# Performance work log

Measured on AMD Instinct MI355X. Metric: run time of the kernel, lower is better.

Reference implementation:

```python
import jax, jax.numpy as jnp
import numpy as np

N = 4096      # nodes
F = 64        # feature dim (= in = hidden = out channels)
DEPTH = 3
RATIO = 0.5


def _gcn(x, A, W, b):
    # GCNConv(improved=True): self-loop weight 2.0, sym-normalized propagation
    n = A.shape[0]
    A_hat = A + 2.0 * jnp.eye(n, dtype=A.dtype)
    deg = A_hat.sum(axis=1)
    dinv = jnp.where(deg > 0, jax.lax.rsqrt(deg), 0.0)
    A_norm = dinv[:, None] * A_hat * dinv[None, :]
    return A_norm @ (x @ W) + b


def _augment(A):
    # add_self_loops (fill 1.0) -> spspmm(A,A) -> remove_self_loops, dense form
    n = A.shape[0]
    eye = jnp.eye(n, dtype=A.dtype)
    A_sl = A + eye
    A2 = A_sl @ A_sl
    return A2 * (1.0 - eye)


def _topk_pool(x, A, p, ratio):
    # TopKPooling: score = tanh((x @ p)/||p||); keep top ceil(ratio*N) nodes
    score = jnp.tanh((x @ p) / jnp.linalg.norm(p))
    k = int(np.ceil(ratio * x.shape[0]))          # static
    vals, perm = jax.lax.top_k(score, k)
    x_new = x[perm] * vals[:, None]
    A_new = A[perm][:, perm]                      # filter_adj
    return x_new, A_new, perm


def setup_inputs() -> dict:
    key = jax.random.key(0)
    ks = jax.random.split(key, 9)
    x = jax.random.normal(ks[0], (N, F), dtype=jnp.float32)
    # sparse random undirected graph, avg degree ~32, no self loops
    u = jax.random.uniform(ks[1], (N, N), dtype=jnp.float32)
    m = (u < (16.0 / N)).astype(jnp.float32)
    adj = jnp.maximum(m, m.T) * (1.0 - jnp.eye(N, dtype=jnp.float32))
    s = 1.0 / np.sqrt(F)
    down_W = jax.random.normal(ks[2], (DEPTH + 1, F, F), dtype=jnp.float32) * s
    down_b = jnp.zeros((DEPTH + 1, F), dtype=jnp.float32)
    pool_w = jax.random.normal(ks[3], (DEPTH, F), dtype=jnp.float32) * s
    up_W = jax.random.normal(ks[4], (DEPTH, F, F), dtype=jnp.float32) * s
    up_b = jnp.zeros((DEPTH, F), dtype=jnp.float32)
    fc_w = jax.random.normal(ks[5], (F, 1), dtype=jnp.float32) * s
    fc_b = jnp.zeros((1,), dtype=jnp.float32)
    prob = jnp.zeros((), dtype=jnp.float32)  # dropout p = 0 -> deterministic
    return {"x": x, "adj": adj, "prob": prob, "down_W": down_W,
            "down_b": down_b, "pool_w": pool_w, "up_W": up_W,
            "up_b": up_b, "fc_w": fc_w, "fc_b": fc_b}


def reference(x, adj, prob, down_W, down_b, pool_w, up_W, up_b, fc_w, fc_b):
    act = jax.nn.relu
    A = adj
    h = act(_gcn(x, A, down_W[0], down_b[0]))
    xs, As, perms = [h], [A], []
    for i in range(DEPTH):
        A = _augment(A)
        h, A, perm = _topk_pool(h, A, pool_w[i], RATIO)
        h = act(_gcn(h, A, down_W[i + 1], down_b[i + 1]))
        if i < DEPTH - 1:
            xs.append(h); As.append(A)
        perms.append(perm)
    for i in range(DEPTH):
        j = DEPTH - 1 - i
        res, A, perm = xs[j], As[j], perms[j]
        up = jnp.zeros_like(res).at[perm].set(h)   # scatter unpool
        h = res + up                               # sum_res
        h = _gcn(h, A, up_W[i], up_b[i])
        if i < DEPTH - 1:
            h = act(h)
    h = jax.nn.relu(h)
    h = h / (1.0 - prob)   # dropout with p=prob(=0): all-ones keep mask
    return h @ fc_w + fc_b
```

## Files before the change

### kernel.cpp

```cpp
#include <hip/hip_runtime.h>
#include <cstdint>
#include <cstddef>


typedef float  f4v    __attribute__((ext_vector_type(4)));
typedef float  f32x4  __attribute__((ext_vector_type(4)));
typedef __bf16 bf16x8 __attribute__((ext_vector_type(8)));
typedef __bf16 bf16x4 __attribute__((ext_vector_type(4)));
typedef int    i32x4  __attribute__((ext_vector_type(4)));

#define NN0 4096
#define NN1 2048
#define NN2 1024
#define NN3 512

__global__ __launch_bounds__(256) void k_zs_deg(const float* __restrict__ X,
                                                const float* __restrict__ W,
                                                const float* __restrict__ A,
                                                int n,
                                                float* __restrict__ DEG,
                                                float* __restrict__ zs,
                                                __bf16* __restrict__ ADJB,
                                                __bf16* __restrict__ Zt0,
                                                __bf16* __restrict__ Zt1,
                                                __bf16* __restrict__ Zt2) {
    __shared__ float Ws[64][65];
    __shared__ float Xs[4][64];
    __shared__ float degs[4];
    int tid = threadIdx.x;
#pragma unroll
    for (int q = 0; q < 16; q++) {
        int idx = q * 256 + tid;
        Ws[idx >> 6][idx & 63] = W[idx];
    }
    int row0 = blockIdx.x << 2;
    int r = tid >> 6, lane = tid & 63;
    const float* ar = A + (size_t)(row0 + r) * n;
    __bf16* ab = ADJB + (size_t)(row0 + r) * n;
    float s = 0.f;
    for (int j = lane << 2; j < n; j += 256) {
        f4v a = *(const f4v*)(ar + j);
        s += a[0] + a[1] + a[2] + a[3];
        bf16x4 b;
#pragma unroll
        for (int e = 0; e < 4; e++) b[e] = (__bf16)a[e];
        *(bf16x4*)(ab + j) = b;
    }
#pragma unroll
    for (int off = 32; off > 0; off >>= 1) s += __shfl_xor(s, off);
    if (lane == 0) { degs[r] = s; DEG[row0 + r] = s; }
    Xs[r][lane] = X[((size_t)(row0 + r) << 6) + lane];
    __syncthreads();
    float acc = 0.f;
#pragma unroll
    for (int k = 0; k < 64; k++) acc = fmaf(Xs[r][k], Ws[k][lane], acc);
    float di = 1.0f / sqrtf(degs[r] + 2.0f);
    float zval = di * acc;
    zs[((size_t)(row0 + r) << 6) + lane] = zval;
    __syncthreads();
    Xs[r][lane] = zval;
    __syncthreads();
    int c = tid >> 2, rr = tid & 3;
    float v = Xs[rr][c];
    float v0 = (float)(__bf16)v;
    float v1 = (float)(__bf16)(v - v0);
    size_t o = (size_t)c * n + row0 + rr;
    Zt0[o] = (__bf16)v0;
    Zt1[o] = (__bf16)(v - v0);
    Zt2[o] = (__bf16)(v - v0 - v1);
}

__global__ __launch_bounds__(256) void k_zs_pool(const float* __restrict__ H,
                                                 const float* __restrict__ sc,
                                                 const int* __restrict__ perm,
                                                 const float* __restrict__ W,
                                                 const float* __restrict__ deg,
                                                 float* __restrict__ zs,
                                                 __bf16* __restrict__ Zt0,
                                                 __bf16* __restrict__ Zt1,
                                                 __bf16* __restrict__ Zt2,
                                                 int n) {
    __shared__ float Ws[64][65];
    __shared__ float Xs[4][64];
    int tid = threadIdx.x;
#pragma unroll
    for (int q = 0; q < 16; q++) {
        int idx = q * 256 + tid;
        Ws[idx >> 6][idx & 63] = W[idx];
    }
    int row0 = blockIdx.x << 2;
    int r = tid >> 6, f = tid & 63;
    int src = perm[row0 + r];
    Xs[r][f] = H[((size_t)src << 6) + f] * sc[src];
    __syncthreads();
    float acc = 0.f;
#pragma unroll
    for (int k = 0; k < 64; k++) acc = fmaf(Xs[r][k], Ws[k][f], acc);
    float di = 1.0f / sqrtf(deg[row0 + r] + 2.0f);
    float zval = di * acc;
    zs[((size_t)(row0 + r) << 6) + f] = zval;
    if (Zt0) {
        __syncthreads();
        Xs[r][f] = zval;
        __syncthreads();
        int c = tid >> 2, rr = tid & 3;
        float v = Xs[rr][c];
        float v0 = (float)(__bf16)v;
        float v1 = (float)(__bf16)(v - v0);
        size_t o = (size_t)c * n + row0 + rr;
        Zt0[o] = (__bf16)v0;
        Zt1[o] = (__bf16)(v - v0);
        if (Zt2) Zt2[o] = (__bf16)(v - v0 - v1);
    }
}

__global__ __launch_bounds__(256) void k_zs_unpool(const float* __restrict__ RES,
                                                   const float* __restrict__ HS,
                                                   const int* __restrict__ inv,
                                                   const float* __restrict__ W,
                                                   const float* __restrict__ deg,
                                                   float* __restrict__ zs,
                                                   __bf16* __restrict__ Zt0,
                                                   __bf16* __restrict__ Zt1,
                                                   __bf16* __restrict__ Zt2,
                                                   int n) {
    __shared__ float Ws[64][65];
    __shared__ float Xs[4][64];
    int tid = threadIdx.x;
#pragma unroll
    for (int q = 0; q < 16; q++) {
        int idx = q * 256 + tid;
        Ws[idx >> 6][idx & 63] = W[idx];
    }
    int row0 = blockIdx.x << 2;
    int r = tid >> 6, f = tid & 63;
    int grow = row0 + r;
    int iv = inv[grow];
    float xv = RES[((size_t)grow << 6) + f];
    if (iv >= 0) xv += HS[((size_t)iv << 6) + f];
    Xs[r][f] = xv;
    __syncthreads();
    float acc = 0.f;
#pragma unroll
    for (int k = 0; k < 64; k++) acc = fmaf(Xs[r][k], Ws[k][f], acc);
    float di = 1.0f / sqrtf(deg[grow] + 2.0f);
    float zval = di * acc;
    zs[((size_t)grow << 6) + f] = zval;
    if (Zt0) {
        __syncthreads();
        Xs[r][f] = zval;
        __syncthreads();
        int c = tid >> 2, rr = tid & 3;
        float v = Xs[rr][c];
        float v0 = (float)(__bf16)v;
        float v1 = (float)(__bf16)(v - v0);
        size_t o = (size_t)c * n + row0 + rr;
        Zt0[o] = (__bf16)v0;
        Zt1[o] = (__bf16)(v - v0);
        if (Zt2) Zt2[o] = (__bf16)(v - v0 - v1);
    }
}

__global__ __launch_bounds__(256) void k_prop(const float* __restrict__ A,
                                              const float* __restrict__ zs,
                                              float* __restrict__ ypart, int n) {
    int rb = blockIdx.x, ks = blockIdx.y;
    int chunk = n >> 2;
    int j0 = ks * chunk;
    __shared__ float AtT[64][68];
    __shared__ float Zt[64][68];
    int tid = threadIdx.x;
    int lr = tid >> 2;
    int lc = (tid & 3) << 4;
    int ty = tid >> 4, tx = tid & 15;
    float acc[4][4] = {};
    const float* Arow = A + (size_t)(rb * 64 + lr) * n;
    for (int jt = j0; jt < j0 + chunk; jt += 64) {
#pragma unroll
        for (int q = 0; q < 4; q++) {
            f4v av = *(const f4v*)(Arow + jt + lc + (q << 2));
#pragma unroll
            for (int e = 0; e < 4; e++) AtT[lc + (q << 2) + e][lr] = av[e];
        }
#pragma unroll
        for (int q = 0; q < 4; q++) {
            f4v zv = *(const f4v*)(zs + (((size_t)(jt + lr)) << 6) + lc + (q << 2));
            *(f4v*)&Zt[lr][lc + (q << 2)] = zv;
        }
        __syncthreads();
#pragma unroll 4
        for (int k = 0; k < 64; k++) {
            f4v a4 = *(const f4v*)&AtT[k][ty << 2];
            f4v z4 = *(const f4v*)&Zt[k][tx << 2];
#pragma unroll
            for (int r = 0; r < 4; r++)
#pragma unroll
                for (int c = 0; c < 4; c++)
                    acc[r][c] = fmaf(a4[r], z4[c], acc[r][c]);
        }
        __syncthreads();
    }
    float* yp = ypart + ((size_t)ks * n << 6);
#pragma unroll
    for (int r = 0; r < 4; r++) {
        f4v o; o[0] = acc[r][0]; o[1] = acc[r][1]; o[2] = acc[r][2]; o[3] = acc[r][3];
        *(f4v*)(yp + (((size_t)(rb * 64 + (ty << 2) + r)) << 6) + (tx << 2)) = o;
    }
}

template<int NP>
__global__ __launch_bounds__(256) void k_propm(const __bf16* __restrict__ Zt0,
                                               const __bf16* __restrict__ Zt1,
                                               const __bf16* __restrict__ Zt2,
                                               const __bf16* __restrict__ Ab,
                                               float* __restrict__ ypart,
                                               int n, int chunk) {
    __shared__ __bf16 At[128 * 64];
    __shared__ __bf16 B[NP][64 * 64];
    const __bf16* Zp[3] = {Zt0, Zt1, Zt2};
    int tid = threadIdx.x;
    int m0 = blockIdx.x * 128;
    int k0b = blockIdx.y * chunk;
    int wave = tid >> 6, lane = tid & 63, quad = lane >> 4, l16 = lane & 15;
    int wm = wave << 5;
    f32x4 acc[2][4] = {};
    for (int k0 = k0b; k0 < k0b + chunk; k0 += 64) {
#pragma unroll
        for (int it = 0; it < 4; it++) {
            int e = it * 256 + tid;
            int row = e >> 3, seg = e & 7;
            int sg = seg ^ (row & 7);
            const __bf16* g = Ab + ((size_t)(m0 + row) * n + k0 + (sg << 3));
            __builtin_amdgcn_global_load_lds(
                (const __attribute__((address_space(1))) void*)g,
                (__attribute__((address_space(3))) void*)(At + (e << 3)), 16, 0, 0);
        }
#pragma unroll
        for (int it = 0; it < 2; it++) {
            int e = it * 256 + tid;
            int row = e >> 3, seg = e & 7;
            int sg = seg ^ (row & 7);
            size_t off = (size_t)row * n + k0 + (sg << 3);
#pragma unroll
            for (int p = 0; p < NP; p++)
                __builtin_amdgcn_global_load_lds(
                    (const __attribute__((address_space(1))) void*)(Zp[p] + off),
                    (__attribute__((address_space(3))) void*)(B[p] + (e << 3)), 16, 0, 0);
        }
        __syncthreads();
#pragma unroll
        for (int kk = 0; kk < 2; kk++) {
            int s = (kk << 2) + quad;
            bf16x8 af[2];
#pragma unroll
            for (int im = 0; im < 2; im++) {
                int row = wm + (im << 4) + l16;
                af[im] = *(const bf16x8*)(At + (row << 6) + ((s ^ (row & 7)) << 3));
            }
#pragma unroll
            for (int cg = 0; cg < 4; cg++) {
                int brow = (cg << 4) + l16;
                int so = (s ^ (brow & 7)) << 3;
#pragma unroll
                for (int p = 0; p < NP; p++) {
                    bf16x8 bv = *(const bf16x8*)(B[p] + (brow << 6) + so);
#pragma unroll
                    for (int im = 0; im < 2; im++)
                        acc[im][cg] = __builtin_amdgcn_mfma_f32_16x16x32_bf16(
                            af[im], bv, acc[im][cg], 0, 0, 0);
                }
            }
        }
        __syncthreads();
    }
    float* yp = ypart + ((size_t)blockIdx.y * n << 6);
#pragma unroll
    for (int im = 0; im < 2; im++)
#pragma unroll
        for (int cg = 0; cg < 4; cg++)
#pragma unroll
            for (int r = 0; r < 4; r++) {
                int grow = m0 + wm + (im << 4) + (quad << 2) + r;
                int gcol = (cg << 4) + l16;
                yp[((size_t)grow << 6) + gcol] = acc[im][cg][r];
            }
}

__global__ __launch_bounds__(256) void k_epi(const float* __restrict__ ypart,
                                             const float* __restrict__ zs,
                                             const float* __restrict__ deg,
                                             const float* __restrict__ b,
                                             float* __restrict__ H, int n, int S,
                                             int relu,
                                             const float* __restrict__ p,
                                             float* __restrict__ score,
                                             int* __restrict__ cnt,
                                             const float* __restrict__ fcw,
                                             const float* __restrict__ fcb,
                                             const float* __restrict__ prob,
                                             float* __restrict__ out) {
    int idx = blockIdx.x * 256 + threadIdx.x;
    int i = idx >> 6, f = idx & 63;
    size_t stride = (size_t)n << 6;
    float y = 0.f;
    for (int s2 = 0; s2 < S; s2++) y += ypart[(size_t)s2 * stride + idx];
    float di = 1.0f / sqrtf(deg[i] + 2.0f);
    float v = di * (y + 2.0f * zs[idx]) + b[f];
    if (relu) v = fmaxf(v, 0.f);
    if (H) H[idx] = v;
    if (p) {
        float pv = p[f];
        float d = v * pv, q = pv * pv;
#pragma unroll
        for (int off = 32; off > 0; off >>= 1) {
            d += __shfl_xor(d, off);
            q += __shfl_xor(q, off);
        }
        if (f == 0) score[i] = tanhf(d / sqrtf(q));
        if (idx < n) cnt[idx] = 0;
    }
    if (fcw) {
        float hv = fmaxf(v, 0.f) * fcw[f];
#pragma unroll
        for (int off = 32; off > 0; off >>= 1) hv += __shfl_xor(hv, off);
        if (f == 0) out[i] = hv / (1.0f - prob[0]) + fcb[0];
    }
}

__global__ __launch_bounds__(256) void k_topk_count(const float* __restrict__ score,
                                                    int* __restrict__ cnt, int n) {
    __shared__ float sc[256];
    int j0 = blockIdx.y * 256;
    sc[threadIdx.x] = score[j0 + threadIdx.x];
    int i = blockIdx.x * 256 + threadIdx.x;
    float si = score[i];
    __syncthreads();
    int c = 0;
#pragma unroll 8
    for (int t = 0; t < 256; t++) {
        float sj = sc[t];
        int j = j0 + t;
        c += ((sj > si) || (sj == si && j < i)) ? 1 : 0;
    }
    atomicAdd(&cnt[i], c);
}
__global__ __launch_bounds__(256) void k_topk_scatter(const int* __restrict__ cnt,
                                                      int* __restrict__ perm,
                                                      int* __restrict__ inv,
                                                      float* __restrict__ degN,
                                                      int k) {
    int i = blockIdx.x * 256 + threadIdx.x;
    int c = cnt[i];
    if (c < k) perm[c] = i;
    inv[i] = (c < k) ? c : -1;
    if (i < k) degN[i] = 0.f;
}

__global__ __launch_bounds__(256) void k_gather8b(const __bf16* __restrict__ Ab,
                                                  const int* __restrict__ perm,
                                                  signed char* __restrict__ Mg,
                                                  int kbits4 ) {
    size_t idx16 = (size_t)blockIdx.x * 256 + threadIdx.x;
    int r = (int)(idx16 >> kbits4);
    int c = ((int)idx16 & ((1 << kbits4) - 1)) << 4;
    int K = 1 << (kbits4 + 4);
    int src = perm[r];
    const __bf16* rowp = Ab + (size_t)src * K + c;
    bf16x8 a0 = *(const bf16x8*)rowp;
    bf16x8 a1 = *(const bf16x8*)(rowp + 8);
    union { signed char ch[16]; i32x4 v; } u;
#pragma unroll
    for (int j = 0; j < 8; j++) {
        float val = (float)a0[j];
        if (src == c + j) val += 1.0f;
        u.ch[j] = (signed char)val;
    }
#pragma unroll
    for (int j = 0; j < 8; j++) {
        float val = (float)a1[j];
        if (src == c + 8 + j) val += 1.0f;
        u.ch[8 + j] = (signed char)val;
    }
    *(i32x4*)(Mg + (idx16 << 4)) = u.v;
}

__global__ __launch_bounds__(256) void k_gather(const float* __restrict__ A,
                                                const int* __restrict__ perm,
                                                __bf16* __restrict__ Mg,
                                                int kbits3 ) {
    size_t idx8 = (size_t)blockIdx.x * 256 + threadIdx.x;
    int r = (int)(idx8 >> kbits3);
    int c = ((int)idx8 & ((1 << kbits3) - 1)) << 3;
    int K = 1 << (kbits3 + 3);
    int src = perm[r];
    const float* rowp = A + (size_t)src * K + c;
    f4v v0 = *(const f4v*)rowp;
    f4v v1 = *(const f4v*)(rowp + 4);
    bf16x8 t;
#pragma unroll
    for (int j = 0; j < 4; j++) {
        float v = v0[j]; if (src == c + j) v += 1.0f; t[j] = (__bf16)v;
    }
#pragma unroll
    for (int j = 0; j < 4; j++) {
        float v = v1[j]; if (src == c + 4 + j) v += 1.0f; t[4 + j] = (__bf16)v;
    }
    *(bf16x8*)(Mg + idx8 * 8) = t;
}

template<int BN>
__global__ __launch_bounds__(256) void k_augmm_i8(const signed char* __restrict__ Mg,
                                                  float* __restrict__ C,
                                                  __bf16* __restrict__ Cb,
                                                  float* __restrict__ DEG,
                                                  int nk, int K) {
    __shared__ signed char At[64 * 128];
    __shared__ signed char Bt[BN * 128];
    constexpr int NI = BN / 32;
    int tid = threadIdx.x;
    int m0 = blockIdx.x * 64, n0 = blockIdx.y * BN;
    int wave = tid >> 6, lane = tid & 63;
    int wm = (wave >> 1) << 5;
    int wn = (wave & 1) * (BN >> 1);
    int quad = lane >> 4, l16 = lane & 15;
    i32x4 acc[2][NI] = {};
    for (int k0 = 0; k0 < K; k0 += 128) {
#pragma unroll
        for (int it = 0; it < 2; it++) {
            int e = it * 256 + tid;
            int row = e >> 3, cs = e & 7;
            int cg = cs ^ (row & 7);
            const signed char* g = Mg + ((size_t)(m0 + row) * K + k0 + (cg << 4));
            __builtin_amdgcn_global_load_lds(
                (const __attribute__((address_space(1))) void*)g,
                (__attribute__((address_space(3))) void*)(At + (e << 4)), 16, 0, 0);
        }
#pragma unroll
        for (int it = 0; it < BN / 32; it++) {
            int e = it * 256 + tid;
            int row = e >> 3, cs = e & 7;
            int cg = cs ^ (row & 7);
            const signed char* g = Mg + ((size_t)(n0 + row) * K + k0 + (cg << 4));
            __builtin_amdgcn_global_load_lds(
                (const __attribute__((address_space(1))) void*)g,
                (__attribute__((address_space(3))) void*)(Bt + (e << 4)), 16, 0, 0);
        }
        __syncthreads();
#pragma unroll
        for (int h = 0; h < 2; h++) {
            int cix = (h << 2) + quad;
            i32x4 af[2], bf[NI];
#pragma unroll
            for (int im = 0; im < 2; im++) {
                int row = wm + (im << 4) + l16;
                af[im] = *(const i32x4*)(At + (row << 7) + ((cix ^ (row & 7)) << 4));
            }
#pragma unroll
            for (int in2 = 0; in2 < NI; in2++) {
                int row = wn + (in2 << 4) + l16;
                bf[in2] = *(const i32x4*)(Bt + (row << 7) + ((cix ^ (row & 7)) << 4));
            }
#pragma unroll
            for (int im = 0; im < 2; im++)
#pragma unroll
                for (int in2 = 0; in2 < NI; in2++)
                    acc[im][in2] = __builtin_amdgcn_mfma_i32_16x16x64_i8(
                        af[im], bf[in2], acc[im][in2], 0, 0, 0);
        }
        __syncthreads();
    }
#pragma unroll
    for (int im = 0; im < 2; im++) {
#pragma unroll
        for (int r = 0; r < 4; r++) {
            int grow = m0 + wm + (im << 4) + (quad << 2) + r;
            int part = 0;
#pragma unroll
            for (int in2 = 0; in2 < NI; in2++) {
                int gcol = n0 + wn + (in2 << 4) + l16;
                int v = (grow == gcol) ? 0 : acc[im][in2][r];
                if (C)  C[(size_t)grow * nk + gcol] = (float)v;
                if (Cb) Cb[(size_t)grow * nk + gcol] = (__bf16)(float)v;
                part += v;
            }
#pragma unroll
            for (int off = 8; off > 0; off >>= 1) part += __shfl_xor(part, off);
            if (l16 == 0) atomicAdd(&DEG[grow], (float)part);
        }
    }
}

__global__ __launch_bounds__(256) void k_augmm_bf(const __bf16* __restrict__ Mg,
                                                  float* __restrict__ C,
                                                  float* __restrict__ DEG,
                                                  int nk, int K) {
    constexpr int BN = 64;
    __shared__ __bf16 At[64 * 64];
    __shared__ __bf16 Bt[BN * 64];
    constexpr int NI = BN / 32;
    int tid = threadIdx.x;
    int m0 = blockIdx.x * 64, n0 = blockIdx.y * BN;
    int wave = tid >> 6, lane = tid & 63;
    int wm = (wave >> 1) << 5;
    int wn = (wave & 1) * (BN >> 1);
    int quad = lane >> 4, l16 = lane & 15;
    f32x4 acc[2][NI] = {};
    for (int k0 = 0; k0 < K; k0 += 64) {
#pragma unroll
        for (int it = 0; it < 2; it++) {
            int e = it * 256 + tid;
            int row = e >> 3, seg = e & 7;
            int sg = seg ^ (row & 7);
            const __bf16* g = Mg + ((size_t)(m0 + row) * K + k0 + (sg << 3));
            __builtin_amdgcn_global_load_lds(
                (const __attribute__((address_space(1))) void*)g,
                (__attribute__((address_space(3))) void*)(At + (e << 3)), 16, 0, 0);
        }
#pragma unroll
        for (int it = 0; it < BN / 32; it++) {
            int e = it * 256 + tid;
            int row = e >> 3, seg = e & 7;
            int sg = seg ^ (row & 7);
            const __bf16* g = Mg + ((size_t)(n0 + row) * K + k0 + (sg << 3));
            __builtin_amdgcn_global_load_lds(
                (const __attribute__((address_space(1))) void*)g,
                (__attribute__((address_space(3))) void*)(Bt + (e << 3)), 16, 0, 0);
        }
        __syncthreads();
#pragma unroll
        for (int kk = 0; kk < 2; kk++) {
            int s = (kk << 2) + quad;
            bf16x8 af[2], bfm[NI];
#pragma unroll
            for (int im = 0; im < 2; im++) {
                int row = wm + (im << 4) + l16;
                af[im] = *(const bf16x8*)(At + (row << 6) + ((s ^ (row & 7)) << 3));
            }
#pragma unroll
            for (int in2 = 0; in2 < NI; in2++) {
                int row = wn + (in2 << 4) + l16;
                bfm[in2] = *(const bf16x8*)(Bt + (row << 6) + ((s ^ (row & 7)) << 3));
            }
#pragma unroll
            for (int im = 0; im < 2; im++)
#pragma unroll
                for (int in2 = 0; in2 < NI; in2++)
                    acc[im][in2] = __builtin_amdgcn_mfma_f32_16x16x32_bf16(
                        af[im], bfm[in2], acc[im][in2], 0, 0, 0);
        }
        __syncthreads();
    }
#pragma unroll
    for (int im = 0; im < 2; im++) {
#pragma unroll
        for (int r = 0; r < 4; r++) {
            int grow = m0 + wm + (im << 4) + (quad << 2) + r;
            float part = 0.f;
#pragma unroll
            for (int in2 = 0; in2 < NI; in2++) {
                int gcol = n0 + wn + (in2 << 4) + l16;
                float v = (grow == gcol) ? 0.f : acc[im][in2][r];
                C[(size_t)grow * nk + gcol] = v;
                part += v;
            }
#pragma unroll
            for (int off = 8; off > 0; off >>= 1) part += __shfl_xor(part, off);
            if (l16 == 0) atomicAdd(&DEG[grow], part);
        }
    }
}

extern "C" void kernel_launch(void* const* d_in, const int* in_sizes, int n_in,
                              void* d_out, int out_size, void* d_ws, size_t ws_size,
                              hipStream_t stream) {
    (void)in_sizes; (void)n_in; (void)out_size;
    const float* x     = (const float*)d_in[0];
    const float* adj   = (const float*)d_in[1];
    const float* prob  = (const float*)d_in[2];
    const float* downW = (const float*)d_in[3];
    const float* downb = (const float*)d_in[4];
    const float* poolw = (const float*)d_in[5];
    const float* upW   = (const float*)d_in[6];
    const float* upb   = (const float*)d_in[7];
    const float* fcw   = (const float*)d_in[8];
    const float* fcb   = (const float*)d_in[9];

    char* ws = (char*)d_ws;
    signed char* MG8 = (signed char*)(ws + 0);
    __bf16* MGB  = (__bf16*)(ws + 0);
    float*  A2   = (float*)(ws + 25165824);
    float*  A3   = (float*)(ws + 29360128);
    __bf16* ADJB = (__bf16*)(ws + 30408704);
    __bf16* A1B  = (__bf16*)(ws + 63963136);
    float*  H0   = (float*)(ws + 72351744);
    float*  H1   = (float*)(ws + 73400320);
    float*  H2   = (float*)(ws + 73924608);
    float*  H3   = (float*)(ws + 74186752);
    float*  ZS   = (float*)(ws + 74317824);
    __bf16* ZT0  = (__bf16*)(ws + 75366400);
    __bf16* ZT1  = (__bf16*)(ws + 75890688);
    __bf16* ZT2  = (__bf16*)(ws + 76414976);
    float*  YP   = (float*)(ws + 76939264);
    float*  UA   = (float*)(ws + 93716480);
    float*  UB   = (float*)(ws + 94240768);
    float*  DEG0 = (float*)(ws + 94765056);
    float*  DEG1 = (float*)(ws + 94781440);
    float*  DEG2 = (float*)(ws + 94789632);
    float*  DEG3 = (float*)(ws + 94793728);
    float*  SCORE= (float*)(ws + 94795776);
    int*    PERM0= (int*)(ws + 94812160);
    int*    PERM1= (int*)(ws + 94820352);
    int*    PERM2= (int*)(ws + 94824448);
    int*    INV0 = (int*)(ws + 94826496);
    int*    INV1 = (int*)(ws + 94842880);
    int*    INV2 = (int*)(ws + 94851072);
    int*    CNT  = (int*)(ws + 94855168);
    if (ws_size < (size_t)94871552) return;

    k_zs_deg<<<NN0 / 4, 256, 0, stream>>>(x, downW, adj, NN0, DEG0, ZS,
                                          ADJB, ZT0, ZT1, ZT2);
    k_propm<3><<<dim3(NN0 / 128, 16), 256, 0, stream>>>(ZT0, ZT1, ZT2, ADJB, YP, NN0, 256);
    k_epi<<<NN0 / 4, 256, 0, stream>>>(YP, ZS, DEG0, downb, H0, NN0, 16, 1,
                                       poolw + 0, SCORE, CNT,
                                       nullptr, nullptr, nullptr, nullptr);
    k_topk_count<<<dim3(NN0 / 256, NN0 / 256), 256, 0, stream>>>(SCORE, CNT, NN0);
    k_topk_scatter<<<NN0 / 256, 256, 0, stream>>>(CNT, PERM0, INV0, DEG1, NN1);
    k_gather8b<<<(NN1 * NN0 / 16) / 256, 256, 0, stream>>>(ADJB, PERM0, MG8, 8);
    k_augmm_i8<128><<<dim3(NN1 / 64, NN1 / 128), 256, 0, stream>>>(MG8, nullptr, A1B, DEG1, NN1, NN0);
    k_zs_pool<<<NN1 / 4, 256, 0, stream>>>(H0, SCORE, PERM0, downW + 4096, DEG1, ZS,
                                           ZT0, ZT1, ZT2, NN1);
    k_propm<3><<<dim3(NN1 / 128, 32), 256, 0, stream>>>(ZT0, ZT1, ZT2, A1B, YP, NN1, 64);
    k_epi<<<NN1 / 4, 256, 0, stream>>>(YP, ZS, DEG1, downb + 64, H1, NN1, 32, 1,
                                       poolw + 64, SCORE, CNT,
                                       nullptr, nullptr, nullptr, nullptr);
    k_topk_count<<<dim3(NN1 / 256, NN1 / 256), 256, 0, stream>>>(SCORE, CNT, NN1);
    k_topk_scatter<<<NN1 / 256, 256, 0, stream>>>(CNT, PERM1, INV1, DEG2, NN2);
    k_gather8b<<<(NN2 * NN1 / 16) / 256, 256, 0, stream>>>(A1B, PERM1, MG8, 7);
    k_augmm_i8<64><<<dim3(NN2 / 64, NN2 / 64), 256, 0, stream>>>(MG8, A2, nullptr, DEG2, NN2, NN1);
    k_zs_pool<<<NN2 / 4, 256, 0, stream>>>(H1, SCORE, PERM1, downW + 2 * 4096, DEG2, ZS,
                                           nullptr, nullptr, nullptr, NN2);
    k_prop<<<dim3(NN2 / 64, 4), 256, 0, stream>>>(A2, ZS, YP, NN2);
    k_epi<<<NN2 / 4, 256, 0, stream>>>(YP, ZS, DEG2, downb + 2 * 64, H2, NN2, 4, 1,
                                       poolw + 128, SCORE, CNT,
                                       nullptr, nullptr, nullptr, nullptr);
    k_topk_count<<<dim3(NN2 / 256, NN2 / 256), 256, 0, stream>>>(SCORE, CNT, NN2);
    k_topk_scatter<<<NN2 / 256, 256, 0, stream>>>(CNT, PERM2, INV2, DEG3, NN3);
    k_gather<<<(NN3 * NN2 / 8) / 256, 256, 0, stream>>>(A2, PERM2, MGB, 7);
    k_augmm_bf<<<dim3(NN3 / 64, NN3 / 64), 256, 0, stream>>>(MGB, A3, DEG3, NN3, NN2);
    k_zs_pool<<<NN3 / 4, 256, 0, stream>>>(H2, SCORE, PERM2, downW + 3 * 4096, DEG3, ZS,
                                           nullptr, nullptr, nullptr, NN3);
    k_prop<<<dim3(NN3 / 64, 4), 256, 0, stream>>>(A3, ZS, YP, NN3);
    k_epi<<<NN3 / 4, 256, 0, stream>>>(YP, ZS, DEG3, downb + 3 * 64, H3, NN3, 4, 1,
                                       nullptr, nullptr, nullptr,
                                       nullptr, nullptr, nullptr, nullptr);

    k_zs_unpool<<<NN2 / 4, 256, 0, stream>>>(H2, H3, INV2, upW, DEG2, ZS,
                                             nullptr, nullptr, nullptr, NN2);
    k_prop<<<dim3(NN2 / 64, 4), 256, 0, stream>>>(A2, ZS, YP, NN2);
    k_epi<<<NN2 / 4, 256, 0, stream>>>(YP, ZS, DEG2, upb, UA, NN2, 4, 1,
                                       nullptr, nullptr, nullptr,
                                       nullptr, nullptr, nullptr, nullptr);
    k_zs_unpool<<<NN1 / 4, 256, 0, stream>>>(H1, UA, INV1, upW + 4096, DEG1, ZS,
                                             ZT0, ZT1, nullptr, NN1);
    k_propm<2><<<dim3(NN1 / 128, 32), 256, 0, stream>>>(ZT0, ZT1, nullptr, A1B, YP, NN1, 64);
    k_epi<<<NN1 / 4, 256, 0, stream>>>(YP, ZS, DEG1, upb + 64, UB, NN1, 32, 1,
                                       nullptr, nullptr, nullptr,
                                       nullptr, nullptr, nullptr, nullptr);
    k_zs_unpool<<<NN0 / 4, 256, 0, stream>>>(H0, UB, INV0, upW + 2 * 4096, DEG0, ZS,
                                             ZT0, ZT1, nullptr, NN0);
    k_propm<2><<<dim3(NN0 / 128, 16), 256, 0, stream>>>(ZT0, ZT1, nullptr, ADJB, YP, NN0, 256);
    k_epi<<<NN0 / 4, 256, 0, stream>>>(YP, ZS, DEG0, upb + 2 * 64, nullptr, NN0, 16, 0,
                                       nullptr, nullptr, nullptr,
                                       fcw, fcb, prob, (float*)d_out);
}
```

Measured before the change: 364.8 us.

## Replace first-level dense augment GEMM with sparse neighbor-pair scatter

While converting the adjacency to bf16, the first kernel now records each row's neighbor list. The first augment step, a dense int8 GEMM over a gathered 2048x4096 matrix, is replaced by a sparse build: zero a float count matrix, then for every node scatter-add 1 to each pair of its kept neighbors (plus itself) with atomics, and convert the result to bf16 with the diagonal removed. This is meant to remove a dense O(n^2 k) product in favour of work proportional to degree squared. In exchange it adds atomic contention, a fixed 128-entry per-row neighbor cap, and extra zero and convert passes. Separately, the smaller dense propagation kernels now split K into more chunks for more parallelism.

```diff
diff --git a/kernel.cpp b/kernel.cpp
--- a/kernel.cpp
+++ b/kernel.cpp
@@ -21,22 +21,29 @@
                                                 float* __restrict__ DEG,
                                                 float* __restrict__ zs,
                                                 __bf16* __restrict__ ADJB,
+                                                int* __restrict__ NBR,
+                                                int* __restrict__ NCNT,
                                                 __bf16* __restrict__ Zt0,
                                                 __bf16* __restrict__ Zt1,
                                                 __bf16* __restrict__ Zt2) {
     __shared__ float Ws[64][65];
     __shared__ float Xs[4][64];
     __shared__ float degs[4];
+    __shared__ int lcnt[4];
     int tid = threadIdx.x;
 #pragma unroll
     for (int q = 0; q < 16; q++) {
         int idx = q * 256 + tid;
         Ws[idx >> 6][idx & 63] = W[idx];
     }
+    if (tid < 4) lcnt[tid] = 0;
+    __syncthreads();
     int row0 = blockIdx.x << 2;
     int r = tid >> 6, lane = tid & 63;
-    const float* ar = A + (size_t)(row0 + r) * n;
-    __bf16* ab = ADJB + (size_t)(row0 + r) * n;
+    int grow = row0 + r;
+    const float* ar = A + (size_t)grow * n;
+    __bf16* ab = ADJB + (size_t)grow * n;
+    int* nbr = NBR + ((size_t)grow << 7);
     float s = 0.f;
     for (int j = lane << 2; j < n; j += 256) {
         f4v a = *(const f4v*)(ar + j);
@@ -45,18 +52,24 @@
 #pragma unroll
         for (int e = 0; e < 4; e++) b[e] = (__bf16)a[e];
         *(bf16x4*)(ab + j) = b;
+#pragma unroll
+        for (int e = 0; e < 4; e++)
+            if (a[e] != 0.0f) {
+                int slot = atomicAdd(&lcnt[r], 1);
+                nbr[slot] = j + e;
+            }
     }
 #pragma unroll
     for (int off = 32; off > 0; off >>= 1) s += __shfl_xor(s, off);
-    if (lane == 0) { degs[r] = s; DEG[row0 + r] = s; }
-    Xs[r][lane] = X[((size_t)(row0 + r) << 6) + lane];
+    if (lane == 0) { degs[r] = s; DEG[grow] = s; NCNT[grow] = lcnt[r]; }
+    Xs[r][lane] = X[((size_t)grow << 6) + lane];
     __syncthreads();
     float acc = 0.f;
 #pragma unroll
     for (int k = 0; k < 64; k++) acc = fmaf(Xs[r][k], Ws[k][lane], acc);
     float di = 1.0f / sqrtf(degs[r] + 2.0f);
     float zval = di * acc;
-    zs[((size_t)(row0 + r) << 6) + lane] = zval;
+    zs[((size_t)grow << 6) + lane] = zval;
     __syncthreads();
     Xs[r][lane] = zval;
     __syncthreads();
@@ -163,10 +176,10 @@
 
 __global__ __launch_bounds__(256) void k_prop(const float* __restrict__ A,
                                               const float* __restrict__ zs,
-                                              float* __restrict__ ypart, int n) {
-    int rb = blockIdx.x, ks = blockIdx.y;
-    int chunk = n >> 2;
-    int j0 = ks * chunk;
+                                              float* __restrict__ ypart,
+                                              int n, int chunk) {
+    int rb = blockIdx.x;
+    int j0 = blockIdx.y * chunk;
     __shared__ float AtT[64][68];
     __shared__ float Zt[64][68];
     int tid = threadIdx.x;
@@ -200,7 +213,7 @@
         }
         __syncthreads();
     }
-    float* yp = ypart + ((size_t)ks * n << 6);
+    float* yp = ypart + ((size_t)blockIdx.y * n << 6);
 #pragma unroll
     for (int r = 0; r < 4; r++) {
         f4v o; o[0] = acc[r][0]; o[1] = acc[r][1]; o[2] = acc[r][2]; o[3] = acc[r][3];
@@ -356,6 +369,61 @@
     if (i < k) degN[i] = 0.f;
 }
 
+__global__ __launch_bounds__(256) void k_zero4(float* __restrict__ p) {
+    size_t i = ((size_t)blockIdx.x * 256 + threadIdx.x) << 2;
+    *(f4v*)(p + i) = (f4v){0.f, 0.f, 0.f, 0.f};
+}
+__global__ __launch_bounds__(256) void k_pairs(const int* __restrict__ NBR,
+                                               const int* __restrict__ NCNT,
+                                               const int* __restrict__ inv,
+                                               float* __restrict__ C,
+                                               float* __restrict__ DEG,
+                                               int nk) {
+    __shared__ int P[4][132];
+    __shared__ int pm[4];
+    int wave = threadIdx.x >> 6, lane = threadIdx.x & 63;
+    int k = (blockIdx.x << 2) + wave;
+    if (lane == 0) pm[wave] = 0;
+    __syncthreads();
+    int cnt = NCNT[k];
+    const int* nbr = NBR + ((size_t)k << 7);
+    for (int t = lane; t < cnt; t += 64) {
+        int iu = inv[nbr[t]];
+        if (iu >= 0) { int s = atomicAdd(&pm[wave], 1); P[wave][s] = iu; }
+    }
+    if (lane == 0) {
+        int ik = inv[k];
+        if (ik >= 0) { int s = atomicAdd(&pm[wave], 1); P[wave][s] = ik; }
+    }
+    __syncthreads();
+    int m = pm[wave];
+    float fm1 = (float)(m - 1);
+    for (int i = 0; i < m; i++) {
+        int a = P[wave][i];
+        float* crow = C + (size_t)a * nk;
+        for (int j = lane; j < m; j += 64)
+            atomicAdd(&crow[P[wave][j]], 1.0f);
+    }
+    for (int t = lane; t < m; t += 64)
+        atomicAdd(&DEG[P[wave][t]], fm1);
+}
+__global__ __launch_bounds__(256) void k_cvt(const float* __restrict__ C,
+                                             __bf16* __restrict__ Cb,
+                                             int nkbits) {
+    size_t i = ((size_t)blockIdx.x * 256 + threadIdx.x) << 2;
+    int r = (int)(i >> nkbits);
+    int c = (int)(i & (((size_t)1 << nkbits) - 1));
+    f4v v = *(const f4v*)(C + i);
+    bf16x4 b;
+#pragma unroll
+    for (int e = 0; e < 4; e++) {
+        float x = v[e];
+        if (r == c + e) x = 0.f;
+        b[e] = (__bf16)x;
+    }
+    *(bf16x4*)(Cb + i) = b;
+}
+
 __global__ __launch_bounds__(256) void k_gather8b(const __bf16* __restrict__ Ab,
                                                   const int* __restrict__ perm,
                                                   signed char* __restrict__ Mg,
@@ -586,6 +654,7 @@
     const float* fcb   = (const float*)d_in[9];
 
     char* ws = (char*)d_ws;
+    float*  CF   = (float*)(ws + 0);
     signed char* MG8 = (signed char*)(ws + 0);
     __bf16* MGB  = (__bf16*)(ws + 0);
     float*  A2   = (float*)(ws + 25165824);
@@ -615,18 +684,21 @@
     int*    INV1 = (int*)(ws + 94842880);
     int*    INV2 = (int*)(ws + 94851072);
     int*    CNT  = (int*)(ws + 94855168);
-    if (ws_size < (size_t)94871552) return;
+    int*    NBR  = (int*)(ws + 94871552);
+    int*    NCNT = (int*)(ws + 96968704);
+    if (ws_size < (size_t)96985088) return;
 
     k_zs_deg<<<NN0 / 4, 256, 0, stream>>>(x, downW, adj, NN0, DEG0, ZS,
-                                          ADJB, ZT0, ZT1, ZT2);
+                                          ADJB, NBR, NCNT, ZT0, ZT1, ZT2);
     k_propm<3><<<dim3(NN0 / 128, 16), 256, 0, stream>>>(ZT0, ZT1, ZT2, ADJB, YP, NN0, 256);
     k_epi<<<NN0 / 4, 256, 0, stream>>>(YP, ZS, DEG0, downb, H0, NN0, 16, 1,
                                        poolw + 0, SCORE, CNT,
                                        nullptr, nullptr, nullptr, nullptr);
     k_topk_count<<<dim3(NN0 / 256, NN0 / 256), 256, 0, stream>>>(SCORE, CNT, NN0);
     k_topk_scatter<<<NN0 / 256, 256, 0, stream>>>(CNT, PERM0, INV0, DEG1, NN1);
-    k_gather8b<<<(NN1 * NN0 / 16) / 256, 256, 0, stream>>>(ADJB, PERM0, MG8, 8);
-    k_augmm_i8<128><<<dim3(NN1 / 64, NN1 / 128), 256, 0, stream>>>(MG8, nullptr, A1B, DEG1, NN1, NN0);
+    k_zero4<<<(NN1 * NN1 / 4) / 256, 256, 0, stream>>>(CF);
+    k_pairs<<<NN0 / 4, 256, 0, stream>>>(NBR, NCNT, INV0, CF, DEG1, NN1);
+    k_cvt<<<(NN1 * NN1 / 4) / 256, 256, 0, stream>>>(CF, A1B, 11);
     k_zs_pool<<<NN1 / 4, 256, 0, stream>>>(H0, SCORE, PERM0, downW + 4096, DEG1, ZS,
                                            ZT0, ZT1, ZT2, NN1);
     k_propm<3><<<dim3(NN1 / 128, 32), 256, 0, stream>>>(ZT0, ZT1, ZT2, A1B, YP, NN1, 64);
@@ -639,8 +711,8 @@
     k_augmm_i8<64><<<dim3(NN2 / 64, NN2 / 64), 256, 0, stream>>>(MG8, A2, nullptr, DEG2, NN2, NN1);
     k_zs_pool<<<NN2 / 4, 256, 0, stream>>>(H1, SCORE, PERM1, downW + 2 * 4096, DEG2, ZS,
                                            nullptr, nullptr, nullptr, NN2);
-    k_prop<<<dim3(NN2 / 64, 4), 256, 0, stream>>>(A2, ZS, YP, NN2);
-    k_epi<<<NN2 / 4, 256, 0, stream>>>(YP, ZS, DEG2, downb + 2 * 64, H2, NN2, 4, 1,
+    k_prop<<<dim3(NN2 / 64, 16), 256, 0, stream>>>(A2, ZS, YP, NN2, 64);
+    k_epi<<<NN2 / 4, 256, 0, stream>>>(YP, ZS, DEG2, downb + 2 * 64, H2, NN2, 16, 1,
                                        poolw + 128, SCORE, CNT,
                                        nullptr, nullptr, nullptr, nullptr);
     k_topk_count<<<dim3(NN2 / 256, NN2 / 256), 256, 0, stream>>>(SCORE, CNT, NN2);
@@ -649,15 +721,15 @@
     k_augmm_bf<<<dim3(NN3 / 64, NN3 / 64), 256, 0, stream>>>(MGB, A3, DEG3, NN3, NN2);
     k_zs_pool<<<NN3 / 4, 256, 0, stream>>>(H2, SCORE, PERM2, downW + 3 * 4096, DEG3, ZS,
                                            nullptr, nullptr, nullptr, NN3);
-    k_prop<<<dim3(NN3 / 64, 4), 256, 0, stream>>>(A3, ZS, YP, NN3);
-    k_epi<<<NN3 / 4, 256, 0, stream>>>(YP, ZS, DEG3, downb + 3 * 64, H3, NN3, 4, 1,
+    k_prop<<<dim3(NN3 / 64, 8), 256, 0, stream>>>(A3, ZS, YP, NN3, 64);
+    k_epi<<<NN3 / 4, 256, 0, stream>>>(YP, ZS, DEG3, downb + 3 * 64, H3, NN3, 8, 1,
                                        nullptr, nullptr, nullptr,
                                        nullptr, nullptr, nullptr, nullptr);
 
     k_zs_unpool<<<NN2 / 4, 256, 0, stream>>>(H2, H3, INV2, upW, DEG2, ZS,
                                              nullptr, nullptr, nullptr, NN2);
-    k_prop<<<dim3(NN2 / 64, 4), 256, 0, stream>>>(A2, ZS, YP, NN2);
-    k_epi<<<NN2 / 4, 256, 0, stream>>>(YP, ZS, DEG2, upb, UA, NN2, 4, 1,
+    k_prop<<<dim3(NN2 / 64, 16), 256, 0, stream>>>(A2, ZS, YP, NN2, 64);
+    k_epi<<<NN2 / 4, 256, 0, stream>>>(YP, ZS, DEG2, upb, UA, NN2, 16, 1,
                                        nullptr, nullptr, nullptr,
                                        nullptr, nullptr, nullptr, nullptr);
     k_zs_unpool<<<NN1 / 4, 256, 0, stream>>>(H1, UA, INV1, upW + 4096, DEG1, ZS,
```

New measurement: 400.2 us. +9.7%, slower.
